# Performance work log

Hardware: AMD Instinct MI355X
Metric: run time of the kernel (lower is better)

Reference implementation:

```python
import jax, jax.numpy as jnp
import numpy as np


def _conv1d(x, w, b):
    # x: [N, Cin, L], w: [Cout, Cin, 3], padding=1 (same)
    y = jax.lax.conv_general_dilated(x, w, (1,), ((1, 1),),
                                     dimension_numbers=('NCH', 'OIH', 'NCH'))
    return y + b[None, :, None]


def _pool2(x):
    n, c, l = x.shape
    return x.reshape(n, c, l // 2, 2).max(-1)


def _forward(x, w_init, b_init, c1w, c1b, c2w, c2b, c3w, c3b,
             Wx, bx, Wh, bh, Wxo, bxo, Wq, bq, Wk, bk, Wv, bv,
             Wao, bao, Wout, bout):
    B, MEL, T = x.shape
    H = Wxo.shape[0]
    D = Wao.shape[1]
    # --- FeatureExtractor ---
    f = jnp.transpose(x, (0, 2, 1))                 # [B,T,MEL]
    f = jax.nn.relu(f @ w_init.T + b_init)          # [B,T,4L]
    f = f.reshape(B * T, 1, -1)                     # [B*T,1,4L]
    f = _pool2(jax.nn.relu(_conv1d(f, c1w, c1b)))   # [B*T,16,2L]
    f = _pool2(jax.nn.relu(_conv1d(f, c2w, c2b)))   # [B*T,32,L]
    f = _conv1d(f, c3w, c3b)                        # [B*T,1,L] (no relu after conv3)
    f = f.reshape(B, T, -1)                         # [B,T,L]
    scale = 1.0 / jnp.sqrt(jnp.asarray(D, x.dtype))
    def step(carry, x_t):
        c, h = carry
        # fused gate computation: g-order = (i, f, g, o)
        g = (jnp.einsum('gol,bl->bgo', Wx, x_t) + bx
             + jnp.einsum('goh,bh->bgo', Wh, h) + bh)  # [B,4,H]
        i_g = jax.nn.sigmoid(g[:, 0])
        f_g = jax.nn.sigmoid(g[:, 1])
        g_g = jnp.tanh(g[:, 2])
        o_g = jax.nn.sigmoid(g[:, 3])
        c = f_g * c + i_g * g_g
        x_o = jax.nn.sigmoid(x_t @ Wxo.T + bxo)       # [B,H]
        q = (x_o @ Wq.T + bq).reshape(B, H, D)
        k = (c @ Wk.T + bk).reshape(B, H, D)
        v = (o_g @ Wv.T + bv).reshape(B, H, D)
        attn = jax.nn.softmax(jnp.einsum('bhd,bgd->bhg', q, k) * scale, axis=-1)
        ao = jnp.einsum('bhg,bgd->bhd', attn, v)      # [B,H,D]
        h = ao @ Wao[0] + bao[0]                      # [B,H]
        y = h @ Wout.T + bout                         # [B,C]
        return (c, h), y
    c0 = jnp.zeros((B, H), x.dtype)
    h0 = jnp.zeros((B, H), x.dtype)
    _, ys = jax.lax.scan(step, (c0, h0), jnp.transpose(f, (1, 0, 2)))  # [T,B,C]
    return jnp.transpose(ys, (1, 2, 0))               # [B,C,T]


def setup_inputs() -> dict:
    key = jax.random.key(0)
    ks = jax.random.split(key, 16)
    B, MEL, T, L, H, C, D = 8, 128, 64, 256, 256, 10, 256
    s = 0.02
    inp = {}
    inp['x'] = jax.random.normal(ks[0], (B, MEL, T), jnp.float32)
    inp['w_init'] = jax.random.normal(ks[1], (4 * L, MEL), jnp.float32) * s
    inp['b_init'] = jnp.zeros((4 * L,), jnp.float32)
    inp['c1w'] = jax.random.normal(ks[2], (16, 1, 3), jnp.float32) * s
    inp['c1b'] = jnp.zeros((16,), jnp.float32)
    inp['c2w'] = jax.random.normal(ks[3], (32, 16, 3), jnp.float32) * s
    inp['c2b'] = jnp.zeros((32,), jnp.float32)
    inp['c3w'] = jax.random.normal(ks[4], (1, 32, 3), jnp.float32) * s
    inp['c3b'] = jnp.zeros((1,), jnp.float32)
    inp['Wx'] = jax.random.normal(ks[5], (4, H, L), jnp.float32) * s
    inp['bx'] = jnp.zeros((4, H), jnp.float32)
    inp['Wh'] = jax.random.normal(ks[6], (4, H, H), jnp.float32) * s
    inp['bh'] = jnp.zeros((4, H), jnp.float32)
    inp['Wxo'] = jax.random.normal(ks[7], (H, L), jnp.float32) * s
    inp['bxo'] = jnp.zeros((H,), jnp.float32)
    inp['Wq'] = jax.random.normal(ks[8], (H * D, H), jnp.float32) * s
    inp['bq'] = jnp.zeros((H * D,), jnp.float32)
    inp['Wk'] = jax.random.normal(ks[9], (H * D, H), jnp.float32) * s
    inp['bk'] = jnp.zeros((H * D,), jnp.float32)
    inp['Wv'] = jax.random.normal(ks[10], (H * D, H), jnp.float32) * s
    inp['bv'] = jnp.zeros((H * D,), jnp.float32)
    inp['Wao'] = jax.random.normal(ks[11], (1, D), jnp.float32) * s
    inp['bao'] = jnp.zeros((1,), jnp.float32)
    inp['Wout'] = jax.random.normal(ks[12], (C, H), jnp.float32) * s
    inp['bout'] = jnp.zeros((C,), jnp.float32)
    return inp


def reference(x, w_init, b_init, c1w, c1b, c2w, c2b, c3w, c3b,
              Wx, bx, Wh, bh, Wxo, bxo, Wq, bq, Wk, bk, Wv, bv,
              Wao, bao, Wout, bout):
    return _forward(x, w_init, b_init, c1w, c1b, c2w, c2b, c3w, c3b,
                    Wx, bx, Wh, bh, Wxo, bxo, Wq, bq, Wk, bk, Wv, bv,
                    Wao, bao, Wout, bout)
```

## Files before the change

kernel.cpp:

```cpp
#include <hip/hip_runtime.h>
#include <hip/hip_fp16.h>
#include <math.h>

#define WS_XIN   0L
#define WS_GF    65536L
#define WS_STATS 65536L
#define WS_BARS  98304L
#define WS_FS    589824L
#define WS_XO    720896L
#define WS_GX    851968L
#define WS_Q     1376256L
#define WS_WKH   18153472L
#define WS_WVE   34930688L
#define WS_BVE   34996224L
#define WS_KT    34996480L
#define WS_HH    35520768L
#define WS_C     35653888L
#define WS_OG    35655936L
#define WS_VW    35657984L

#define NBLK 256

typedef unsigned long long u64;

__device__ __forceinline__ float sigmf(float x){ return 1.0f/(1.0f + expf(-x)); }
__device__ __forceinline__ float dot4(float4 a, float4 b){
  return a.x*b.x + a.y*b.y + a.z*b.z + a.w*b.w;
}
__device__ __forceinline__ void h8_to_f8(uint4 v, float4& a, float4& b){
  const __half2* hp = (const __half2*)&v;
  float2 f0 = __half22float2(hp[0]);
  float2 f1 = __half22float2(hp[1]);
  float2 f2 = __half22float2(hp[2]);
  float2 f3 = __half22float2(hp[3]);
  a = make_float4(f0.x, f0.y, f1.x, f1.y);
  b = make_float4(f2.x, f2.y, f3.x, f3.y);
}
__device__ __forceinline__ float4 h4_to_f4(uint2 v){
  const __half2* hp = (const __half2*)&v;
  float2 f0 = __half22float2(hp[0]);
  float2 f1 = __half22float2(hp[1]);
  return make_float4(f0.x, f0.y, f1.x, f1.y);
}

__device__ __forceinline__ float cld(const float* p){
  return __hip_atomic_load((float*)p, __ATOMIC_RELAXED, __HIP_MEMORY_SCOPE_AGENT);
}
__device__ __forceinline__ void cst(float* p, float v){
  __hip_atomic_store(p, v, __ATOMIC_RELAXED, __HIP_MEMORY_SCOPE_AGENT);
}
__device__ __forceinline__ float2 cld2(const float* p){
  u64 v = __hip_atomic_load((const u64*)p, __ATOMIC_RELAXED, __HIP_MEMORY_SCOPE_AGENT);
  float2 r;
  r.x = __uint_as_float((unsigned)(v & 0xffffffffu));
  r.y = __uint_as_float((unsigned)(v >> 32));
  return r;
}
__device__ __forceinline__ void cst2(float* p, float a, float b){
  u64 v = ((u64)__float_as_uint(b) << 32) | (u64)__float_as_uint(a);
  __hip_atomic_store((u64*)p, v, __ATOMIC_RELAXED, __HIP_MEMORY_SCOPE_AGENT);
}

__device__ __forceinline__ void gbar(unsigned* bar, unsigned ph){
  __syncthreads();
  if (threadIdx.x == 0){
    const unsigned g = blockIdx.x & 31u;
    asm volatile("s_waitcnt vmcnt(0)" ::: "memory");
    unsigned old = __hip_atomic_fetch_add(&bar[g*64], 1u, __ATOMIC_RELAXED, __HIP_MEMORY_SCOPE_AGENT);
    if (old == ph*8u - 1u){
      unsigned t = __hip_atomic_fetch_add(&bar[2048], 1u, __ATOMIC_RELAXED, __HIP_MEMORY_SCOPE_AGENT);
      if (t == ph*32u - 1u)
        __hip_atomic_store(&bar[2112], ph, __ATOMIC_RELAXED, __HIP_MEMORY_SCOPE_AGENT);
    }
    if (blockIdx.x < 32){
      while (__hip_atomic_load(&bar[2112], __ATOMIC_RELAXED, __HIP_MEMORY_SCOPE_AGENT) < ph)
        __builtin_amdgcn_s_sleep(2);
      __hip_atomic_store(&bar[2176 + blockIdx.x*64], ph, __ATOMIC_RELAXED, __HIP_MEMORY_SCOPE_AGENT);
    } else {
      while (__hip_atomic_load(&bar[2176 + g*64], __ATOMIC_RELAXED, __HIP_MEMORY_SCOPE_AGENT) < ph)
        __builtin_amdgcn_s_sleep(2);
    }
  }
  __syncthreads();
}

__launch_bounds__(256)
__global__ void k_init(const float* __restrict__ x, float* __restrict__ ws){
  int i = blockIdx.x*256 + threadIdx.x;
  int r = i >> 7, m = i & 127;
  int t = r >> 3, b = r & 7;
  ws[WS_XIN + i] = x[b*8192 + m*64 + t];
  if (i < 2048){ ws[WS_HH + i] = 0.f; ws[WS_C + i] = 0.f; }
}

__launch_bounds__(256)
__global__ void k_wk16(const float* __restrict__ in, __half* __restrict__ out){
  size_t i = ((size_t)blockIdx.x*256 + threadIdx.x)*8;
  float4 a = *(const float4*)(in + i);
  float4 b = *(const float4*)(in + i + 4);
  uint4 v;
  __half2* vp = (__half2*)&v;
  vp[0] = __floats2half2_rn(a.x, a.y);
  vp[1] = __floats2half2_rn(a.z, a.w);
  vp[2] = __floats2half2_rn(b.x, b.y);
  vp[3] = __floats2half2_rn(b.z, b.w);
  *(uint4*)(out + i) = v;
}

__launch_bounds__(256)
__global__ void k_gemm_nt(const float* __restrict__ W, const float* __restrict__ X,
                          const float* __restrict__ b1, const float* __restrict__ b2,
                          float* __restrict__ out, int M, int K, int act){
  __shared__ float Wt[32*132];
  __shared__ float Xt[32*132];
  const int tid = threadIdx.x;
  const int tx = tid & 15, ty = tid >> 4;
  const int m0 = blockIdx.x * 128, n0 = blockIdx.y * 128;
  float acc[8][8];
  #pragma unroll
  for (int i = 0; i < 8; i++)
    #pragma unroll
    for (int j = 0; j < 8; j++) acc[i][j] = 0.f;

  for (int k0 = 0; k0 < K; k0 += 32){
    #pragma unroll
    for (int i = 0; i < 4; i++){
      int f4 = i*256 + tid;
      int row = f4 >> 3;
      int j4 = (f4 & 7) * 4;
      float4 w = *(const float4*)&W[(size_t)(m0+row)*K + k0 + j4];
      Wt[(j4+0)*132 + row] = w.x;
      Wt[(j4+1)*132 + row] = w.y;
      Wt[(j4+2)*132 + row] = w.z;
      Wt[(j4+3)*132 + row] = w.w;
      float4 xv = *(const float4*)&X[(size_t)(n0+row)*K + k0 + j4];
      Xt[(j4+0)*132 + row] = xv.x;
      Xt[(j4+1)*132 + row] = xv.y;
      Xt[(j4+2)*132 + row] = xv.z;
      Xt[(j4+3)*132 + row] = xv.w;
    }
    __syncthreads();
    for (int k = 0; k < 32; k++){
      float4 a0 = *(const float4*)&Wt[k*132 + 4*tx];
      float4 a1 = *(const float4*)&Wt[k*132 + 64 + 4*tx];
      float4 x0 = *(const float4*)&Xt[k*132 + 4*ty];
      float4 x1 = *(const float4*)&Xt[k*132 + 64 + 4*ty];
      float am[8] = {a0.x,a0.y,a0.z,a0.w,a1.x,a1.y,a1.z,a1.w};
      float xn[8] = {x0.x,x0.y,x0.z,x0.w,x1.x,x1.y,x1.z,x1.w};
      #pragma unroll
      for (int mi = 0; mi < 8; mi++)
        #pragma unroll
        for (int ni = 0; ni < 8; ni++)
          acc[mi][ni] += am[mi]*xn[ni];
    }
    __syncthreads();
  }

  float bvv[8];
  #pragma unroll
  for (int mi = 0; mi < 8; mi++){
    int m = m0 + ((mi < 4) ? (4*tx + mi) : (64 + 4*tx + mi - 4));
    float bb = b1[m];
    if (b2) bb += b2[m];
    bvv[mi] = bb;
  }
  #pragma unroll
  for (int ni = 0; ni < 8; ni++){
    int n = n0 + ((ni < 4) ? (4*ty + ni) : (64 + 4*ty + ni - 4));
    float v[8];
    #pragma unroll
    for (int mi = 0; mi < 8; mi++){
      float q = acc[mi][ni] + bvv[mi];
      if (act == 1) q = fmaxf(q, 0.f);
      else if (act == 2) q = 1.0f/(1.0f + expf(-q));
      v[mi] = q;
    }
    if (act == 3){
      __half* outh = (__half*)out;
      uint2 u0, u1;
      __half2* up0 = (__half2*)&u0;
      __half2* up1 = (__half2*)&u1;
      up0[0] = __floats2half2_rn(v[0], v[1]);
      up0[1] = __floats2half2_rn(v[2], v[3]);
      up1[0] = __floats2half2_rn(v[4], v[5]);
      up1[1] = __floats2half2_rn(v[6], v[7]);
      *(uint2*)&outh[(size_t)n*M + m0 + 4*tx]      = u0;
      *(uint2*)&outh[(size_t)n*M + m0 + 64 + 4*tx] = u1;
    } else {
      *(float4*)&out[(size_t)n*M + m0 + 4*tx]      = make_float4(v[0],v[1],v[2],v[3]);
      *(float4*)&out[(size_t)n*M + m0 + 64 + 4*tx] = make_float4(v[4],v[5],v[6],v[7]);
    }
  }
}

__launch_bounds__(256)
__global__ void k_feconv(const float* __restrict__ gf, const float* __restrict__ c1w,
                         const float* __restrict__ c1b, const float* __restrict__ c2w,
                         const float* __restrict__ c2b, const float* __restrict__ c3w,
                         const float* __restrict__ c3b, float* __restrict__ fs){
  __shared__ float fc[1024];
  __shared__ float p1[16*512];
  __shared__ float p2[32*256];
  __shared__ float w1[48], w2[1536], w3[96], bb1[16], bb2[32];
  const int r = blockIdx.x, tid = threadIdx.x;
  #pragma unroll
  for (int i = 0; i < 4; i++) fc[i*256 + tid] = gf[(size_t)r*1024 + i*256 + tid];
  if (tid < 48) w1[tid] = c1w[tid];
  if (tid < 16) bb1[tid] = c1b[tid];
  for (int i = tid; i < 1536; i += 256) w2[i] = c2w[i];
  if (tid < 32) bb2[tid] = c2b[tid];
  if (tid < 96) w3[tid] = c3w[tid];
  __syncthreads();
  for (int i = 0; i < 32; i++){
    int idx = i*256 + tid;
    int ch = idx >> 9, p = idx & 511;
    float k0 = w1[ch*3], k1 = w1[ch*3+1], k2 = w1[ch*3+2], bias = bb1[ch];
    int q = 2*p;
    float xm1 = (q >= 1) ? fc[q-1] : 0.f;
    float x0 = fc[q];
    float x1 = fc[q+1];
    float x2 = (q+2 < 1024) ? fc[q+2] : 0.f;
    float a0 = bias + k0*xm1 + k1*x0 + k2*x1;
    float a1 = bias + k0*x0 + k1*x1 + k2*x2;
    p1[ch*512 + p] = fmaxf(fmaxf(a0, 0.f), fmaxf(a1, 0.f));
  }
  __syncthreads();
  for (int i = 0; i < 32; i++){
    int idx = i*256 + tid;
    int ch = idx >> 8, p = idx & 255;
    float a0 = bb2[ch], a1 = bb2[ch];
    int q = 2*p;
    #pragma unroll
    for (int ci = 0; ci < 16; ci++){
      const float* wp = &w2[(ch*16+ci)*3];
      const float* ip = &p1[ci*512];
      float xm1 = (q >= 1) ? ip[q-1] : 0.f;
      float x0 = ip[q];
      float x1 = ip[q+1];
      float x2 = (q+2 < 512) ? ip[q+2] : 0.f;
      a0 += wp[0]*xm1 + wp[1]*x0 + wp[2]*x1;
      a1 += wp[0]*x0  + wp[1]*x1 + wp[2]*x2;
    }
    p2[ch*256 + p] = fmaxf(fmaxf(a0, 0.f), fmaxf(a1, 0.f));
  }
  __syncthreads();
  if (tid < 256){
    float a = c3b[0];
    const int l = tid;
    #pragma unroll
    for (int ci = 0; ci < 32; ci++){
      const float* wp = &w3[ci*3];
      const float* ip = &p2[ci*256];
      float xm1 = (l >= 1) ? ip[l-1] : 0.f;
      float x0 = ip[l];
      float x2 = (l+1 < 256) ? ip[l+1] : 0.f;
      a += wp[0]*xm1 + wp[1]*x0 + wp[2]*x2;
    }
    fs[(size_t)r*256 + l] = a;
  }
}

__launch_bounds__(256)
__global__ void k_wveff(const float* __restrict__ Wv, const float* __restrict__ bvq,
                        const float* __restrict__ Wao, float* __restrict__ wve,
                        float* __restrict__ bve, unsigned* __restrict__ bar){
  __shared__ float wa[256];
  const int g = blockIdx.x, tid = threadIdx.x;
  if (g == 0){
    for (int i = tid; i < 8192; i += 256) bar[i] = 0u;
  }
  wa[tid] = Wao[tid];
  __syncthreads();
  float acc = 0.f;
  for (int d = 0; d < 256; d++)
    acc += Wv[((size_t)(g*256 + d))*256 + tid] * wa[d];
  wve[g*256 + tid] = acc;
  if (tid == 0){
    float s = 0.f;
    for (int d = 0; d < 256; d++) s += bvq[g*256 + d]*wa[d];
    bve[g] = s;
  }
}

__global__ __launch_bounds__(512, 2)
void k_loop(const float* __restrict__ gx, const float* __restrict__ Wh,
            const __half* __restrict__ wkh, const float* __restrict__ bkb,
            const float* __restrict__ wve, const float* __restrict__ bve,
            const __half* __restrict__ Qh, const float* __restrict__ bao,
            const float* __restrict__ Wout, const float* __restrict__ bout,
            float* __restrict__ c, float* __restrict__ og, float* __restrict__ vw,
            float* __restrict__ Kt, float* __restrict__ stats, float* __restrict__ hH,
            float* __restrict__ y, unsigned* __restrict__ bar){
  __shared__ float S[25088];
  const int blk = blockIdx.x, tid = threadIdx.x;
  unsigned ph = 0;
  const float bao0 = bao[0];

  const int p1_b = blk >> 5, p1_s = blk & 31;
  const int gid  = blk;
  const int p3_b = blk >> 5, p3_ht = (blk >> 2) & 7, p3_gt = blk & 3;
  const int p3_h0 = p3_ht*32, p3_g0 = p3_gt*64;

  float4 whr[4];
  int p1_row;
  {
    const int j = tid >> 4, part = tid & 15;
    const int rr = p1_s*32 + j, o = rr >> 2, gate = rr & 3;
    p1_row = gate*256 + o;
    const float4* wr = (const float4*)(Wh + (size_t)p1_row*256);
    #pragma unroll
    for (int u = 0; u < 4; u++) whr[u] = wr[u*16 + part];
  }

  for (int t = 0; t < 64; t++){
    if (t > 0){
      if (tid < 256){
        const float* sp = stats + ((size_t)p1_b*256 + tid)*16;
        float2 a0 = cld2(sp+0);  float2 b0 = cld2(sp+2);
        float2 a1 = cld2(sp+4);  float2 b1 = cld2(sp+6);
        float2 a2 = cld2(sp+8);  float2 b2 = cld2(sp+10);
        float2 a3 = cld2(sp+12); float2 b3 = cld2(sp+14);
        float m = fmaxf(fmaxf(a0.x, a1.x), fmaxf(a2.x, a3.x));
        float e0 = expf(a0.x - m), e1 = expf(a1.x - m), e2 = expf(a2.x - m), e3 = expf(a3.x - m);
        float den = a0.y*e0 + a1.y*e1 + a2.y*e2 + a3.y*e3;
        float num = b0.x*e0 + b1.x*e1 + b2.x*e2 + b3.x*e3;
        float hv = num/den + bao0;
        S[tid] = hv;
        if (p1_s == 0) cst(&hH[(size_t)t*2048 + p1_b*256 + tid], hv);
      }
    } else {
      if (tid < 256) S[tid] = 0.f;
    }
    __syncthreads();
    {
      const int j = tid >> 4, part = tid & 15;
      const float4* h4 = (const float4*)S;
      float a0 = 0.f;
      #pragma unroll
      for (int u = 0; u < 4; u++)
        a0 += dot4(whr[u], h4[u*16 + part]);
      a0 += __shfl_xor(a0, 1);
      a0 += __shfl_xor(a0, 2);
      a0 += __shfl_xor(a0, 4);
      a0 += __shfl_xor(a0, 8);
      if (part == 0) S[256 + j] = a0 + gx[(size_t)(t*8 + p1_b)*1024 + p1_row];
    }
    __syncthreads();
    if (tid < 8){
      const int o_ = p1_s*8 + tid, ci = p1_b*256 + o_;
      float ig = sigmf(S[256 + tid*4 + 0]);
      float fg = sigmf(S[256 + tid*4 + 1]);
      float gg = tanhf(S[256 + tid*4 + 2]);
      float ov = sigmf(S[256 + tid*4 + 3]);
      float cv = cld(&c[ci]);
      cst(&c[ci], fg*cv + ig*gg);
      cst(&og[ci], ov);
    }
    gbar(bar, ++ph);

    {
      int bb0 = tid >> 6, j40 = tid & 63;
      float* dst = &S[bb0*260 + j40*4];
      const float* src = &c[bb0*256 + j40*4];
      float2 v0 = cld2(src);
      float2 v1 = cld2(src+2);
      dst[0] = v0.x; dst[1] = v0.y; dst[2] = v1.x; dst[3] = v1.y;
    }
    __syncthreads();
    if (tid < 64){
      const int bb = tid >> 3, part = tid & 7;
      const float4* wv4 = (const float4*)(wve + gid*256);
      float sacc = 0.f;
      #pragma unroll
      for (int u = 0; u < 8; u++){
        float4 w = wv4[part*8 + u];
        const float* op = &og[bb*256 + (part*8 + u)*4];
        float2 o0 = cld2(op);
        float2 o1 = cld2(op+2);
        sacc += w.x*o0.x + w.y*o0.y + w.z*o1.x + w.w*o1.y;
      }
      sacc += __shfl_xor(sacc, 1);
      sacc += __shfl_xor(sacc, 2);
      sacc += __shfl_xor(sacc, 4);
      if (part == 0) cst(&vw[bb*256 + gid], sacc + bve[gid]);
    }
    {
      const float4* cl4 = (const float4*)S;
      #pragma unroll 4
      for (int p = 0; p < 8; p++){
        const int d = p*32 + (tid >> 4), part = tid & 15;
        const __half* wr = wkh + ((size_t)gid*256 + d)*256;
        float4 w0 = h4_to_f4(*(const uint2*)(wr + part*4));
        float4 w1 = h4_to_f4(*(const uint2*)(wr + 64 + part*4));
        float4 w2 = h4_to_f4(*(const uint2*)(wr + 128 + part*4));
        float4 w3 = h4_to_f4(*(const uint2*)(wr + 192 + part*4));
        float acc[8];
        #pragma unroll
        for (int bb = 0; bb < 8; bb++){
          acc[bb] = dot4(w0, cl4[bb*65 + part]) + dot4(w1, cl4[bb*65 + 16 + part])
                  + dot4(w2, cl4[bb*65 + 32 + part]) + dot4(w3, cl4[bb*65 + 48 + part]);
        }
        #pragma unroll
        for (int bb = 0; bb < 8; bb++){
          acc[bb] += __shfl_xor(acc[bb], 1);
          acc[bb] += __shfl_xor(acc[bb], 2);
          acc[bb] += __shfl_xor(acc[bb], 4);
          acc[bb] += __shfl_xor(acc[bb], 8);
        }
        const float bkv = bkb[gid*256 + d];
        if (part < 8)
          cst(&Kt[(size_t)part*65536 + gid*256 + d], acc[part] + bkv);
      }
    }
    gbar(bar, ++ph);

    {
      const __half* Qb = Qh + ((size_t)(t*8 + p3_b))*65536 + (size_t)p3_h0*256;
      #pragma unroll
      for (int i = 0; i < 2; i++){
        int f8 = i*512 + tid;
        int hh = f8 >> 5, j8 = f8 & 31;
        uint4 v = *(const uint4*)(Qb + hh*256 + j8*8);
        float4 a, b;
        h8_to_f8(v, a, b);
        float* dst = &S[hh*260 + j8*8];
        *(float4*)dst = a;
        *(float4*)(dst+4) = b;
      }
      const float* Kb = Kt + (size_t)p3_b*65536 + (size_t)p3_g0*256;
      float* Kl = S + 8320;
      #pragma unroll
      for (int i = 0; i < 8; i++){
        int f4 = i*512 + tid;
        int gg = f4 >> 6, j4 = (f4 & 63)*4;
        float* dst = &Kl[gg*260 + j4];
        const float* src = &Kb[gg*256 + j4];
        float2 v0 = cld2(src);
        float2 v1 = cld2(src+2);
        dst[0] = v0.x; dst[1] = v0.y; dst[2] = v1.x; dst[3] = v1.y;
      }
      if (tid < 64) S[24960 + tid] = cld(&vw[p3_b*256 + p3_g0 + tid]);
      __syncthreads();
      const int kh = tid >> 7, r = tid & 127, ty = r >> 4, txl = r & 15;
      float acc[4][4];
      #pragma unroll
      for (int a = 0; a < 4; a++)
        #pragma unroll
        for (int i = 0; i < 4; i++) acc[a][i] = 0.f;
      const float4* Ql4 = (const float4*)S;
      const float4* Kl4 = (const float4*)(S + 8320);
      for (int k4 = 0; k4 < 16; k4++){
        const int kk = kh*16 + k4;
        float4 qv[4], kv[4];
        #pragma unroll
        for (int a = 0; a < 4; a++) qv[a] = Ql4[(ty + 8*a)*65 + kk];
        #pragma unroll
        for (int i = 0; i < 4; i++) kv[i] = Kl4[(txl + 16*i)*65 + kk];
        #pragma unroll
        for (int a = 0; a < 4; a++)
          #pragma unroll
          for (int i = 0; i < 4; i++)
            acc[a][i] += dot4(qv[a], kv[i]);
      }
      __syncthreads();
      float* Pl = S;
      if (kh > 0){
        #pragma unroll
        for (int a = 0; a < 4; a++)
          #pragma unroll
          for (int i = 0; i < 4; i++)
            Pl[(kh-1)*2048 + r*16 + a*4 + i] = acc[a][i];
      }
      __syncthreads();
      if (kh == 0){
        #pragma unroll
        for (int p = 0; p < 3; p++)
          #pragma unroll
          for (int a = 0; a < 4; a++)
            #pragma unroll
            for (int i = 0; i < 4; i++)
              acc[a][i] += Pl[p*2048 + r*16 + a*4 + i];
        #pragma unroll
        for (int a = 0; a < 4; a++)
          #pragma unroll
          for (int i = 0; i < 4; i++)
            acc[a][i] *= 0.0625f;
        #pragma unroll
        for (int a = 0; a < 4; a++){
          float mx = fmaxf(fmaxf(acc[a][0], acc[a][1]), fmaxf(acc[a][2], acc[a][3]));
          mx = fmaxf(mx, __shfl_xor(mx, 1));
          mx = fmaxf(mx, __shfl_xor(mx, 2));
          mx = fmaxf(mx, __shfl_xor(mx, 4));
          mx = fmaxf(mx, __shfl_xor(mx, 8));
          float den = 0.f, num = 0.f;
          #pragma unroll
          for (int i = 0; i < 4; i++){
            float pv = expf(acc[a][i] - mx);
            den += pv;
            num += pv * S[24960 + txl + 16*i];
          }
          den += __shfl_xor(den, 1); num += __shfl_xor(num, 1);
          den += __shfl_xor(den, 2); num += __shfl_xor(num, 2);
          den += __shfl_xor(den, 4); num += __shfl_xor(num, 4);
          den += __shfl_xor(den, 8); num += __shfl_xor(num, 8);
          if (txl == 0){
            const int h = p3_h0 + ty + 8*a;
            float* sp = &stats[(((size_t)p3_b*256 + h)*4 + p3_gt)*4];
            cst2(sp, mx, den);
            cst(sp+2, num);
          }
        }
      }
    }
    gbar(bar, ++ph);
  }

  if (p1_s == 0 && tid < 256){
    const float* sp = stats + ((size_t)p1_b*256 + tid)*16;
    float2 a0 = cld2(sp+0);  float2 b0 = cld2(sp+2);
    float2 a1 = cld2(sp+4);  float2 b1 = cld2(sp+6);
    float2 a2 = cld2(sp+8);  float2 b2 = cld2(sp+10);
    float2 a3 = cld2(sp+12); float2 b3 = cld2(sp+14);
    float m = fmaxf(fmaxf(a0.x, a1.x), fmaxf(a2.x, a3.x));
    float e0 = expf(a0.x - m), e1 = expf(a1.x - m), e2 = expf(a2.x - m), e3 = expf(a3.x - m);
    float den = a0.y*e0 + a1.y*e1 + a2.y*e2 + a3.y*e3;
    float num = b0.x*e0 + b1.x*e1 + b2.x*e2 + b3.x*e3;
    cst(&hH[(size_t)64*2048 + p1_b*256 + tid], num/den + bao0);
  }
  gbar(bar, ++ph);
  if (blk < 64 && tid < 80){
    const int t2 = blk;
    const int bb2 = tid/10, cc = tid - bb2*10;
    const float* hr = &hH[(size_t)(t2+1)*2048 + bb2*256];
    const float* wr2 = &Wout[cc*256];
    float acc = 0.f;
    for (int u = 0; u < 128; u++){
      float2 h2 = cld2(hr + u*2);
      acc += h2.x*wr2[u*2] + h2.y*wr2[u*2+1];
    }
    y[bb2*640 + cc*64 + t2] = acc + bout[cc];
  }
}

extern "C" void kernel_launch(void* const* d_in, const int* in_sizes, int n_in,
                              void* d_out, int out_size, void* d_ws, size_t ws_size,
                              hipStream_t stream){
  (void)in_sizes; (void)n_in; (void)out_size; (void)ws_size;
  const float* x      = (const float*)d_in[0];
  const float* w_init = (const float*)d_in[1];
  const float* b_init = (const float*)d_in[2];
  const float* c1w    = (const float*)d_in[3];
  const float* c1b    = (const float*)d_in[4];
  const float* c2w    = (const float*)d_in[5];
  const float* c2b    = (const float*)d_in[6];
  const float* c3w    = (const float*)d_in[7];
  const float* c3b    = (const float*)d_in[8];
  const float* Wx     = (const float*)d_in[9];
  const float* bx     = (const float*)d_in[10];
  const float* Wh     = (const float*)d_in[11];
  const float* bh     = (const float*)d_in[12];
  const float* Wxo    = (const float*)d_in[13];
  const float* bxo    = (const float*)d_in[14];
  const float* Wq     = (const float*)d_in[15];
  const float* bq     = (const float*)d_in[16];
  const float* Wk     = (const float*)d_in[17];
  const float* bk_    = (const float*)d_in[18];
  const float* Wv     = (const float*)d_in[19];
  const float* bv     = (const float*)d_in[20];
  const float* Wao    = (const float*)d_in[21];
  const float* bao    = (const float*)d_in[22];
  const float* Wout   = (const float*)d_in[23];
  const float* bout   = (const float*)d_in[24];
  float* y  = (float*)d_out;
  float* ws = (float*)d_ws;

  float* xin   = ws + WS_XIN;
  float* gf    = ws + WS_GF;
  float* stats = ws + WS_STATS;
  unsigned* bar = (unsigned*)(ws + WS_BARS);
  float* fs    = ws + WS_FS;
  float* xo    = ws + WS_XO;
  float* gxp   = ws + WS_GX;
  __half* Qh   = (__half*)(ws + WS_Q);
  __half* wkh  = (__half*)(ws + WS_WKH);
  float* wve   = ws + WS_WVE;
  float* bve   = ws + WS_BVE;
  float* Ktp   = ws + WS_KT;
  float* hH    = ws + WS_HH;
  float* cp    = ws + WS_C;
  float* ogp   = ws + WS_OG;
  float* vwp   = ws + WS_VW;

  k_init<<<256, 256, 0, stream>>>(x, ws);
  k_wk16<<<8192, 256, 0, stream>>>(Wk, wkh);
  k_gemm_nt<<<dim3(8, 4), 256, 0, stream>>>(w_init, xin, b_init, nullptr, gf, 1024, 128, 1);
  k_feconv<<<512, 256, 0, stream>>>(gf, c1w, c1b, c2w, c2b, c3w, c3b, fs);
  k_gemm_nt<<<dim3(2, 4), 256, 0, stream>>>(Wxo, fs, bxo, nullptr, xo, 256, 256, 2);
  k_gemm_nt<<<dim3(8, 4), 256, 0, stream>>>(Wx, fs, bx, bh, gxp, 1024, 256, 0);
  k_wveff<<<256, 256, 0, stream>>>(Wv, bv, Wao, wve, bve, bar);
  k_gemm_nt<<<dim3(512, 4), 256, 0, stream>>>(Wq, xo, bq, nullptr, (float*)Qh, 65536, 256, 3);
  k_loop<<<NBLK, 512, 0, stream>>>(gxp, Wh, wkh, bk_, wve, bve, Qh, bao, Wout, bout,
                                   cp, ogp, vwp, Ktp, stats, hH, y, bar);
}
```

Measured before the change: 2.557 ms.

## Store K in fp16 and restructure K projection to two rows per thread

The per-step K projection now keeps each thread on two output rows across a quarter of the hidden dimension. It rotates its starting chunk to spread LDS accesses, and the cross-lane shuffle reduction drops from four stages to two. K is written to global memory as packed half2 and read back as fp16 in the attention phase. This halves the K traffic through the grid barrier and cuts shuffle work. In exchange it adds fp16 rounding on K and more accumulator registers per thread.

Result: slower. 4.487 ms (+75.4%).

```diff
diff --git a/kernel.cpp b/kernel.cpp
--- a/kernel.cpp
+++ b/kernel.cpp
@@ -59,6 +59,16 @@
 __device__ __forceinline__ void cst2(float* p, float a, float b){
   u64 v = ((u64)__float_as_uint(b) << 32) | (u64)__float_as_uint(a);
   __hip_atomic_store((u64*)p, v, __ATOMIC_RELAXED, __HIP_MEMORY_SCOPE_AGENT);
+}
+__device__ __forceinline__ void csth2(unsigned* p, unsigned v){
+  __hip_atomic_store(p, v, __ATOMIC_RELAXED, __HIP_MEMORY_SCOPE_AGENT);
+}
+__device__ __forceinline__ float4 cldh4(const __half* p){
+  u64 v = __hip_atomic_load((const u64*)p, __ATOMIC_RELAXED, __HIP_MEMORY_SCOPE_AGENT);
+  uint2 uv;
+  uv.x = (unsigned)(v & 0xffffffffu);
+  uv.y = (unsigned)(v >> 32);
+  return h4_to_f4(uv);
 }
 
 __device__ __forceinline__ void gbar(unsigned* bar, unsigned ph){
@@ -289,7 +299,7 @@
             const __half* __restrict__ Qh, const float* __restrict__ bao,
             const float* __restrict__ Wout, const float* __restrict__ bout,
             float* __restrict__ c, float* __restrict__ og, float* __restrict__ vw,
-            float* __restrict__ Kt, float* __restrict__ stats, float* __restrict__ hH,
+            __half* __restrict__ Kth, float* __restrict__ stats, float* __restrict__ hH,
             float* __restrict__ y, unsigned* __restrict__ bar){
   __shared__ float S[25088];
   const int blk = blockIdx.x, tid = threadIdx.x;
@@ -311,6 +321,9 @@
     #pragma unroll
     for (int u = 0; u < 4; u++) whr[u] = wr[u*16 + part];
   }
+
+  const int p2_jq = tid & 3, p2_dp = tid >> 2;
+  const int p2_d0 = p2_dp*2;
 
   for (int t = 0; t < 64; t++){
     if (t > 0){
@@ -386,30 +399,39 @@
     }
     {
       const float4* cl4 = (const float4*)S;
+      const __half* wr0 = wkh + ((size_t)gid*256 + p2_d0)*256 + p2_jq*64;
+      const __half* wr1 = wr0 + 256;
+      float acc0[8], acc1[8];
+      #pragma unroll
+      for (int b = 0; b < 8; b++){ acc0[b] = 0.f; acc1[b] = 0.f; }
       #pragma unroll 4
-      for (int p = 0; p < 8; p++){
-        const int d = p*32 + (tid >> 4), part = tid & 15;
-        const __half* wr = wkh + ((size_t)gid*256 + d)*256;
-        float4 w0 = h4_to_f4(*(const uint2*)(wr + part*4));
-        float4 w1 = h4_to_f4(*(const uint2*)(wr + 64 + part*4));
-        float4 w2 = h4_to_f4(*(const uint2*)(wr + 128 + part*4));
-        float4 w3 = h4_to_f4(*(const uint2*)(wr + 192 + part*4));
-        float acc[8];
-        #pragma unroll
-        for (int bb = 0; bb < 8; bb++){
-          acc[bb] = dot4(w0, cl4[bb*65 + part]) + dot4(w1, cl4[bb*65 + 16 + part])
-                  + dot4(w2, cl4[bb*65 + 32 + part]) + dot4(w3, cl4[bb*65 + 48 + part]);
+      for (int u = 0; u < 16; u++){
+        const int uu = (u + p2_jq) & 15;
+        float4 w0 = h4_to_f4(*(const uint2*)(wr0 + uu*4));
+        float4 w1 = h4_to_f4(*(const uint2*)(wr1 + uu*4));
+        const float4* cb = cl4 + p2_jq*16 + uu;
+        #pragma unroll
+        for (int b = 0; b < 8; b++){
+          float4 c4 = cb[b*65];
+          acc0[b] += dot4(w0, c4);
+          acc1[b] += dot4(w1, c4);
         }
-        #pragma unroll
-        for (int bb = 0; bb < 8; bb++){
-          acc[bb] += __shfl_xor(acc[bb], 1);
-          acc[bb] += __shfl_xor(acc[bb], 2);
-          acc[bb] += __shfl_xor(acc[bb], 4);
-          acc[bb] += __shfl_xor(acc[bb], 8);
+      }
+      #pragma unroll
+      for (int b = 0; b < 8; b++){
+        acc0[b] += __shfl_xor(acc0[b], 1);
+        acc0[b] += __shfl_xor(acc0[b], 2);
+        acc1[b] += __shfl_xor(acc1[b], 1);
+        acc1[b] += __shfl_xor(acc1[b], 2);
+      }
+      if (p2_jq == 0){
+        const float bk0 = bkb[gid*256 + p2_d0];
+        const float bk1 = bkb[gid*256 + p2_d0 + 1];
+        #pragma unroll
+        for (int b = 0; b < 8; b++){
+          __half2 hv = __floats2half2_rn(acc0[b] + bk0, acc1[b] + bk1);
+          csth2((unsigned*)&Kth[(size_t)b*65536 + gid*256 + p2_d0], *(unsigned*)&hv);
         }
-        const float bkv = bkb[gid*256 + d];
-        if (part < 8)
-          cst(&Kt[(size_t)part*65536 + gid*256 + d], acc[part] + bkv);
       }
     }
     gbar(bar, ++ph);
@@ -427,17 +449,14 @@
         *(float4*)dst = a;
         *(float4*)(dst+4) = b;
       }
-      const float* Kb = Kt + (size_t)p3_b*65536 + (size_t)p3_g0*256;
+      const __half* Kbh = Kth + (size_t)p3_b*65536 + (size_t)p3_g0*256;
       float* Kl = S + 8320;
       #pragma unroll
       for (int i = 0; i < 8; i++){
-        int f4 = i*512 + tid;
-        int gg = f4 >> 6, j4 = (f4 & 63)*4;
-        float* dst = &Kl[gg*260 + j4];
-        const float* src = &Kb[gg*256 + j4];
-        float2 v0 = cld2(src);
-        float2 v1 = cld2(src+2);
-        dst[0] = v0.x; dst[1] = v0.y; dst[2] = v1.x; dst[3] = v1.y;
+        int f = i*512 + tid;
+        int gg = f >> 6, c4i = f & 63;
+        float4 v = cldh4(Kbh + gg*256 + c4i*4);
+        *(float4*)&Kl[gg*260 + c4i*4] = v;
       }
       if (tid < 64) S[24960 + tid] = cld(&vw[p3_b*256 + p3_g0 + tid]);
       __syncthreads();
@@ -585,7 +604,7 @@
   __half* wkh  = (__half*)(ws + WS_WKH);
   float* wve   = ws + WS_WVE;
   float* bve   = ws + WS_BVE;
-  float* Ktp   = ws + WS_KT;
+  __half* Kth  = (__half*)(ws + WS_KT);
   float* hH    = ws + WS_HH;
   float* cp    = ws + WS_C;
   float* ogp   = ws + WS_OG;
@@ -600,5 +619,5 @@
   k_wveff<<<256, 256, 0, stream>>>(Wv, bv, Wao, wve, bve, bar);
   k_gemm_nt<<<dim3(512, 4), 256, 0, stream>>>(Wq, xo, bq, nullptr, (float*)Qh, 65536, 256, 3);
   k_loop<<<NBLK, 512, 0, stream>>>(gxp, Wh, wkh, bk_, wve, bve, Qh, bao, Wout, bout,
-                                   cp, ogp, vwp, Ktp, stats, hH, y, bar);
-}
+                                   cp, ogp, vwp, Kth, stats, hH, y, bar);
+}
```
